# Performance work log

Hardware: AMD Instinct MI355X
Metric: run time of the kernel (lower is better)

Reference implementation:

```python
import jax, jax.numpy as jnp
import numpy as np
import math

JULIA_ITERS = 64
ESCAPE_RADIUS = 2.0


def _julia_escape_times(seq_len, c_real, c_imag):
    # Positions mapped to the real segment [-2, 2]; iterate z <- z^2 + c,
    # record (first iteration index where |z| > R) / ITERS, else 1.0.
    x = jnp.linspace(-2.0, 2.0, seq_len)
    zr0 = x
    zi0 = jnp.zeros_like(x)
    escaped0 = jnp.zeros(seq_len, dtype=bool)
    et0 = jnp.ones(seq_len, dtype=x.dtype)
    r2 = ESCAPE_RADIUS * ESCAPE_RADIUS

    def step(carry, it):
        zr, zi, escaped, et = carry
        nzr = zr * zr - zi * zi + c_real
        nzi = 2.0 * zr * zi + c_imag
        # torch breaks out of the loop once escaped -> freeze z afterwards
        zr = jnp.where(escaped, zr, nzr)
        zi = jnp.where(escaped, zi, nzi)
        mag2 = zr * zr + zi * zi
        newly = jnp.logical_and(~escaped, mag2 > r2)
        et = jnp.where(newly, it.astype(et.dtype) / JULIA_ITERS, et)
        escaped = jnp.logical_or(escaped, newly)
        return (zr, zi, escaped, et), None

    (_, _, _, et), _ = jax.lax.scan(step, (zr0, zi0, escaped0, et0), jnp.arange(JULIA_ITERS))
    return et


def setup_inputs() -> dict:
    key = jax.random.key(0)
    kq, kk, kv = jax.random.split(key, 3)
    B, S, D = 4, 8192, 64
    return {
        "query": jax.random.normal(kq, (B, S, D), dtype=jnp.float32),
        "key": jax.random.normal(kk, (B, S, D), dtype=jnp.float32),
        "value": jax.random.normal(kv, (B, S, D), dtype=jnp.float32),
        "julia_c_real": jnp.float32(-0.7),
        "julia_c_imag": jnp.float32(0.27),
        "escape_scale": jnp.float32(1.0),
    }


def reference(query, key, value, julia_c_real, julia_c_imag, escape_scale):
    B, S, D = key.shape
    et = _julia_escape_times(S, julia_c_real, julia_c_imag)            # [S]
    julia_weights = jnp.exp(et * escape_scale)                          # [S]
    bias = jnp.log(julia_weights + 1e-8)                                # [S]
    scores = jnp.einsum("bqd,bkd->bqk", query, key) / math.sqrt(D)     # [B,S,S]
    scores = scores + bias[None, None, :]
    attn = jax.nn.softmax(scores, axis=-1)
    out = jnp.einsum("bqk,bkd->bqd", attn, value)                       # [B,S,D]
    return out  # squeeze(1) is a no-op for S > 1
```

## Files before the change

### kernel.cpp

```cpp
#include <hip/hip_runtime.h>
#include <math.h>

#define S_LEN 8192
#define DHEAD 64
#define NBATCH 4
#define BK 32
#define KIT 64

typedef unsigned short u16;
typedef unsigned int u32;
typedef __attribute__((ext_vector_type(8))) _Float16 half8;
typedef __attribute__((ext_vector_type(2))) __fp16 fp16x2;
typedef __attribute__((ext_vector_type(4))) float f32x4;

union HU8 { int4 i4; half8 h8; u32 w[4]; };
union H2U { fp16x2 h2; u32 w; };
union HU  { _Float16 h; u16 u; };

#if __has_builtin(__builtin_amdgcn_exp2f)
#define EXP2(x) __builtin_amdgcn_exp2f(x)
#else
#define EXP2(x) exp2f(x)
#endif

__device__ __forceinline__ u16 f2h(float f) {
    HU x; x.h = (_Float16)f; return x.u;
}
__device__ __forceinline__ u32 packh2(float a, float b) {
    H2U x; x.h2 = __builtin_amdgcn_cvt_pkrtz(a, b); return x.w;
}

__global__ void prep_kernel(const float* __restrict__ K, const float* __restrict__ V,
                            const float* crp, const float* cip, const float* scp,
                            u16* __restrict__ blob, float* __restrict__ bias2) {
    int bid = blockIdx.x, tid = threadIdx.x;
    if (bid < 1024) {
        int b = bid >> 8, t = bid & 255;
        __shared__ float Kt[32 * 64];
        __shared__ float Vt[32 * 65];
        int row = tid >> 3, c8 = (tid & 7) * 8;
        const float* ks = K + ((size_t)(b * S_LEN + t * 32 + row)) * 64 + c8;
        const float* vs = V + ((size_t)(b * S_LEN + t * 32 + row)) * 64 + c8;
        float4 ka = *(const float4*)ks, kb4 = *(const float4*)(ks + 4);
        float4 va = *(const float4*)vs, vb4 = *(const float4*)(vs + 4);
        *(float4*)&Kt[row * 64 + c8] = ka;
        *(float4*)&Kt[row * 64 + c8 + 4] = kb4;
        float* vr = &Vt[row * 65 + c8];
        vr[0] = va.x; vr[1] = va.y; vr[2] = va.z; vr[3] = va.w;
        vr[4] = vb4.x; vr[5] = vb4.y; vr[6] = vb4.z; vr[7] = vb4.w;
        __syncthreads();

        int j = tid >> 6, lane = tid & 63, low = lane & 15, h = lane >> 4;
        u16* tb = blob + ((size_t)(b * 256 + t)) * 4096;
        {
            int kt = j >> 1, ds = j & 1;
            int krow = 8 * (low >> 2) + 4 * kt + (low & 3);
            const float* src = &Kt[krow * 64 + ds * 32 + h * 8];
            u32 wds[4];
#pragma unroll
            for (int i = 0; i < 4; ++i)
                wds[i] = (u32)f2h(src[2 * i]) | ((u32)f2h(src[2 * i + 1]) << 16);
            *(int4*)(tb + j * 512 + lane * 8) = make_int4(wds[0], wds[1], wds[2], wds[3]);
        }
        {
            int col = j * 16 + low;
            u32 wds[4];
#pragma unroll
            for (int i = 0; i < 4; ++i) {
                float a = Vt[(h * 8 + 2 * i) * 65 + col];
                float c = Vt[(h * 8 + 2 * i + 1) * 65 + col];
                wds[i] = (u32)f2h(a) | ((u32)f2h(c) << 16);
            }
            *(int4*)(tb + 2048 + j * 512 + lane * 8) = make_int4(wds[0], wds[1], wds[2], wds[3]);
        }
    } else {
#pragma clang fp contract(off)
        int i = (bid - 1024) * 256 + tid;
        double cr = (double)crp[0], ci = (double)cip[0], sc = (double)scp[0];
        double step = 4.0 / (double)(S_LEN - 1);
        double x = (i == S_LEN - 1) ? 2.0 : (-2.0 + step * (double)i);
        double zr = x, zi = 0.0, et = 1.0;
        bool esc = false;
        for (int it = 0; it < 64; ++it) {
            double nzr = zr * zr - zi * zi + cr;
            double nzi = 2.0 * zr * zi + ci;
            if (!esc) { zr = nzr; zi = nzi; }
            double m2 = zr * zr + zi * zi;
            if (!esc && m2 > 4.0) { et = (double)it / 64.0; esc = true; }
        }
        double bias = log(exp(et * sc) + 1e-8);
        bias2[i] = (float)(bias * 1.4426950408889634 - 20.0);
    }
}

__global__ __launch_bounds__(256, 2)
void flash_kernel(const float* __restrict__ Q, const u16* __restrict__ blob,
                  const float* __restrict__ bias2, float* __restrict__ Out) {
    __shared__ __align__(16) char smem[17664];

    const int tid = threadIdx.x;
    const int l = tid & 63, low = l & 15, h = l >> 4;
    const int kq = __builtin_amdgcn_readfirstlane(tid >> 6);

    const int bid = blockIdx.x;
    const int batch = bid & 3;
    const int qtile = bid >> 2;
    const int q0 = qtile * 64;

    const float qscale = 0.18033688011112042f;
    half8 qfrag[4][2];
#pragma unroll
    for (int qf = 0; qf < 4; ++qf) {
        const float* qrow = Q + ((size_t)(batch * S_LEN + q0 + qf * 16 + low)) * DHEAD + h * 8;
#pragma unroll
        for (int ds = 0; ds < 2; ++ds) {
            f32x4 a = *(const f32x4*)(qrow + ds * 32);
            f32x4 b = *(const f32x4*)(qrow + ds * 32 + 4);
            HU8 u;
            u.w[0] = packh2(a[0] * qscale, a[1] * qscale);
            u.w[1] = packh2(a[2] * qscale, a[3] * qscale);
            u.w[2] = packh2(b[0] * qscale, b[1] * qscale);
            u.w[3] = packh2(b[2] * qscale, b[3] * qscale);
            qfrag[qf][ds] = u.h8;
        }
    }

    const u16* kvb = blob + ((size_t)(batch * 256 + kq * 64)) * 4096;
    const int loff = l * 8;
    const float* bbase = bias2 + kq * 2048;

    f32x4 o[4][4];
#pragma unroll
    for (int qf = 0; qf < 4; ++qf)
#pragma unroll
        for (int dt = 0; dt < 4; ++dt) o[qf][dt] = (f32x4){0, 0, 0, 0};
    float lsum[4] = {0.f, 0.f, 0.f, 0.f};

    HU8 kf[2][4];
    f32x4 bvv[2][2];
#pragma unroll
    for (int j = 0; j < 4; ++j) kf[0][j].i4 = *(const int4*)(kvb + j * 512 + loff);
    bvv[0][0] = *(const f32x4*)(bbase + h * 8);
    bvv[0][1] = *(const f32x4*)(bbase + h * 8 + 4);

#pragma unroll 2
    for (int ki = 0; ki < KIT; ++ki) {
        const int c = ki & 1;
        const u16* tb = kvb + ki * 4096;

        HU8 vf[4];
#pragma unroll
        for (int j = 0; j < 4; ++j) vf[j].i4 = *(const int4*)(tb + 2048 + j * 512 + loff);

        const u16* tn = tb + 4096;
#pragma unroll
        for (int j = 0; j < 4; ++j) kf[c ^ 1][j].i4 = *(const int4*)(tn + j * 512 + loff);
        const float* bpn = bbase + (ki + 1) * 32 + h * 8;
        bvv[c ^ 1][0] = *(const f32x4*)bpn;
        bvv[c ^ 1][1] = *(const f32x4*)(bpn + 4);

        HU8 pf[4];
#pragma unroll
        for (int kt = 0; kt < 2; ++kt) {
            const f32x4 binit = kt ? bvv[c][1] : bvv[c][0];
            f32x4 st[4];
#pragma unroll
            for (int qf = 0; qf < 4; ++qf) {
                f32x4 a = __builtin_amdgcn_mfma_f32_16x16x32_f16(kf[c][kt * 2].h8, qfrag[qf][0], binit, 0, 0, 0);
                a = __builtin_amdgcn_mfma_f32_16x16x32_f16(kf[c][kt * 2 + 1].h8, qfrag[qf][1], a, 0, 0, 0);
                st[qf] = a;
            }
#pragma unroll
            for (int qf = 0; qf < 4; ++qf) {
                float p0 = EXP2(st[qf][0]), p1 = EXP2(st[qf][1]);
                float p2 = EXP2(st[qf][2]), p3 = EXP2(st[qf][3]);
                lsum[qf] += (p0 + p1) + (p2 + p3);
                pf[qf].w[kt * 2]     = packh2(p0, p1);
                pf[qf].w[kt * 2 + 1] = packh2(p2, p3);
            }
        }

#pragma unroll
        for (int dt = 0; dt < 4; ++dt)
#pragma unroll
            for (int qf = 0; qf < 4; ++qf)
                o[qf][dt] = __builtin_amdgcn_mfma_f32_16x16x32_f16(vf[dt].h8, pf[qf].h8, o[qf][dt], 0, 0, 0);
    }

#pragma unroll
    for (int qf = 0; qf < 4; ++qf) {
        lsum[qf] += __shfl_xor(lsum[qf], 16, 64);
        lsum[qf] += __shfl_xor(lsum[qf], 32, 64);
    }

    float* MO = (float*)smem;
    float* ML = (float*)(smem + 17408);
#pragma unroll 1
    for (int src = 1; src < 4; ++src) {
        __syncthreads();
        if (kq == src) {
#pragma unroll
            for (int qf = 0; qf < 4; ++qf) {
                const int row = qf * 16 + low;
#pragma unroll
                for (int dt = 0; dt < 4; ++dt)
                    *(f32x4*)&MO[row * 68 + dt * 16 + h * 4] = o[qf][dt];
                if (h == 0) ML[row] = lsum[qf];
            }
        }
        __syncthreads();
        if (kq == 0) {
#pragma unroll
            for (int qf = 0; qf < 4; ++qf) {
                const int row = qf * 16 + low;
#pragma unroll
                for (int dt = 0; dt < 4; ++dt) {
                    f32x4 a = *(const f32x4*)&MO[row * 68 + dt * 16 + h * 4];
#pragma unroll
                    for (int jj = 0; jj < 4; ++jj) o[qf][dt][jj] += a[jj];
                }
                lsum[qf] += ML[row];
            }
        }
    }

    if (kq == 0) {
#pragma unroll
        for (int qf = 0; qf < 4; ++qf) {
            const float inv = 1.f / lsum[qf];
            float* orow = Out + ((size_t)(batch * S_LEN + q0 + qf * 16 + low)) * DHEAD;
#pragma unroll
            for (int dt = 0; dt < 4; ++dt) {
                f32x4 r;
#pragma unroll
                for (int jj = 0; jj < 4; ++jj) r[jj] = o[qf][dt][jj] * inv;
                *(f32x4*)(orow + dt * 16 + h * 4) = r;
            }
        }
    }
}

extern "C" void kernel_launch(void* const* d_in, const int* in_sizes, int n_in,
                              void* d_out, int out_size, void* d_ws, size_t ws_size,
                              hipStream_t stream) {
    const float* Q  = (const float*)d_in[0];
    const float* K  = (const float*)d_in[1];
    const float* V  = (const float*)d_in[2];
    const float* cr = (const float*)d_in[3];
    const float* ci = (const float*)d_in[4];
    const float* sc = (const float*)d_in[5];
    float* out = (float*)d_out;

    char* ws = (char*)d_ws;
    float* bias2 = (float*)ws;
    u16*   blob  = (u16*)(ws + 32768);

    prep_kernel<<<dim3(1056), dim3(256), 0, stream>>>(K, V, cr, ci, sc, blob, bias2);
    flash_kernel<<<dim3(512), dim3(256), 0, stream>>>(Q, blob, bias2, out);
}
```

Measured before the change: 149.7 us.

## Split key range across eight waves per block with tree reduction

Doubles the block to 512 threads so eight waves each process half as many key tiles, raising in-block parallelism for the same 512-block grid. The serial three-step merge of partial outputs through shared memory is replaced by a log-depth tree reduction using a larger shared buffer. The larger shared footprint and register pressure under the new launch bounds may limit how many blocks fit per CU and could cause spills.

```diff
diff --git a/kernel.cpp b/kernel.cpp
--- a/kernel.cpp
+++ b/kernel.cpp
@@ -5,7 +5,7 @@
 #define DHEAD 64
 #define NBATCH 4
 #define BK 32
-#define KIT 64
+#define KIT 32
 
 typedef unsigned short u16;
 typedef unsigned int u32;
@@ -93,10 +93,10 @@
     }
 }
 
-__global__ __launch_bounds__(256, 2)
+__global__ __launch_bounds__(512, 4)
 void flash_kernel(const float* __restrict__ Q, const u16* __restrict__ blob,
                   const float* __restrict__ bias2, float* __restrict__ Out) {
-    __shared__ __align__(16) char smem[17664];
+    __shared__ __align__(16) char smem[70656];
 
     const int tid = threadIdx.x;
     const int l = tid & 63, low = l & 15, h = l >> 4;
@@ -125,9 +125,9 @@
         }
     }
 
-    const u16* kvb = blob + ((size_t)(batch * 256 + kq * 64)) * 4096;
+    const u16* kvb = blob + ((size_t)(batch * 256 + kq * 32)) * 4096;
     const int loff = l * 8;
-    const float* bbase = bias2 + kq * 2048;
+    const float* bbase = bias2 + kq * 1024;
 
     f32x4 o[4][4];
 #pragma unroll
@@ -194,37 +194,48 @@
     }
 
     float* MO = (float*)smem;
-    float* ML = (float*)(smem + 17408);
-#pragma unroll 1
-    for (int src = 1; src < 4; ++src) {
-        __syncthreads();
-        if (kq == src) {
-#pragma unroll
-            for (int qf = 0; qf < 4; ++qf) {
-                const int row = qf * 16 + low;
-#pragma unroll
-                for (int dt = 0; dt < 4; ++dt)
-                    *(f32x4*)&MO[row * 68 + dt * 16 + h * 4] = o[qf][dt];
-                if (h == 0) ML[row] = lsum[qf];
-            }
-        }
-        __syncthreads();
-        if (kq == 0) {
-#pragma unroll
-            for (int qf = 0; qf < 4; ++qf) {
-                const int row = qf * 16 + low;
-#pragma unroll
-                for (int dt = 0; dt < 4; ++dt) {
-                    f32x4 a = *(const f32x4*)&MO[row * 68 + dt * 16 + h * 4];
-#pragma unroll
-                    for (int jj = 0; jj < 4; ++jj) o[qf][dt][jj] += a[jj];
-                }
-                lsum[qf] += ML[row];
-            }
-        }
-    }
+    float* ML = (float*)(smem + 69632);
+#define WRITE_REGION(reg)                                                     \
+    do {                                                                      \
+        const int _r = (reg);                                                 \
+        _Pragma("unroll")                                                     \
+        for (int qf = 0; qf < 4; ++qf) {                                      \
+            const int row = qf * 16 + low;                                    \
+            _Pragma("unroll")                                                 \
+            for (int dt = 0; dt < 4; ++dt)                                    \
+                *(f32x4*)&MO[_r * 4352 + row * 68 + dt * 16 + h * 4] = o[qf][dt]; \
+            if (h == 0) ML[_r * 64 + row] = lsum[qf];                         \
+        }                                                                     \
+    } while (0)
+#define ADD_REGION(reg)                                                       \
+    do {                                                                      \
+        const int _r = (reg);                                                 \
+        _Pragma("unroll")                                                     \
+        for (int qf = 0; qf < 4; ++qf) {                                      \
+            const int row = qf * 16 + low;                                    \
+            _Pragma("unroll")                                                 \
+            for (int dt = 0; dt < 4; ++dt) {                                  \
+                f32x4 a = *(const f32x4*)&MO[_r * 4352 + row * 68 + dt * 16 + h * 4]; \
+                _Pragma("unroll")                                             \
+                for (int jj = 0; jj < 4; ++jj) o[qf][dt][jj] += a[jj];        \
+            }                                                                 \
+            lsum[qf] += ML[_r * 64 + row];                                    \
+        }                                                                     \
+    } while (0)
+
+    if (kq >= 4) WRITE_REGION(kq - 4);
+    __syncthreads();
+    if (kq < 4) ADD_REGION(kq);
+    __syncthreads();
+    if (kq == 2 || kq == 3) WRITE_REGION(kq - 2);
+    __syncthreads();
+    if (kq < 2) ADD_REGION(kq);
+    __syncthreads();
+    if (kq == 1) WRITE_REGION(0);
+    __syncthreads();
 
     if (kq == 0) {
+        ADD_REGION(0);
 #pragma unroll
         for (int qf = 0; qf < 4; ++qf) {
             const float inv = 1.f / lsum[qf];
@@ -238,6 +249,8 @@
             }
         }
     }
+#undef WRITE_REGION
+#undef ADD_REGION
 }
 
 extern "C" void kernel_launch(void* const* d_in, const int* in_sizes, int n_in,
@@ -256,5 +269,5 @@
     u16*   blob  = (u16*)(ws + 32768);
 
     prep_kernel<<<dim3(1056), dim3(256), 0, stream>>>(K, V, cr, ci, sc, blob, bias2);
-    flash_kernel<<<dim3(512), dim3(256), 0, stream>>>(Q, blob, bias2, out);
-}
+    flash_kernel<<<dim3(512), dim3(512), 0, stream>>>(Q, blob, bias2, out);
+}
```

New measurement: 569.9 us. +280.7%, slower.

## Split key range across two blocks per query tile and merge partials

Applied to the files above, without the earlier changes.

Doubles the grid so each block handles half the keys for a 64-query tile. Unnormalized partial outputs and row sums go to workspace, and a new merge kernel adds them and normalizes. This targets under-occupancy: 512 blocks at 2 per CU on 256 CUs fills only one wave. In exchange it adds extra global traffic for the partials (about 16 MB written and read) and a third kernel launch. The merge relies on a shared fixed max offset (bias minus 20 in log2 space) so partials can be summed without rescaling.

```diff
diff --git a/kernel.cpp b/kernel.cpp
--- a/kernel.cpp
+++ b/kernel.cpp
@@ -5,7 +5,7 @@
 #define DHEAD 64
 #define NBATCH 4
 #define BK 32
-#define KIT 64
+#define KIT 32
 
 typedef unsigned short u16;
 typedef unsigned int u32;
@@ -95,7 +95,8 @@
 
 __global__ __launch_bounds__(256, 2)
 void flash_kernel(const float* __restrict__ Q, const u16* __restrict__ blob,
-                  const float* __restrict__ bias2, float* __restrict__ Out) {
+                  const float* __restrict__ bias2, float* __restrict__ Ppart,
+                  float* __restrict__ Lpart) {
     __shared__ __align__(16) char smem[17664];
 
     const int tid = threadIdx.x;
@@ -104,7 +105,8 @@
 
     const int bid = blockIdx.x;
     const int batch = bid & 3;
-    const int qtile = bid >> 2;
+    const int khalf = (bid >> 2) & 1;
+    const int qtile = bid >> 3;
     const int q0 = qtile * 64;
 
     const float qscale = 0.18033688011112042f;
@@ -125,9 +127,9 @@
         }
     }
 
-    const u16* kvb = blob + ((size_t)(batch * 256 + kq * 64)) * 4096;
+    const u16* kvb = blob + ((size_t)(batch * 256 + khalf * 128 + kq * 32)) * 4096;
     const int loff = l * 8;
-    const float* bbase = bias2 + kq * 2048;
+    const float* bbase = bias2 + khalf * 4096 + kq * 1024;
 
     f32x4 o[4][4];
 #pragma unroll
@@ -225,19 +227,34 @@
     }
 
     if (kq == 0) {
+        float* pbase = Ppart + (size_t)khalf * (NBATCH * S_LEN * DHEAD);
+        float* lbase = Lpart + (size_t)khalf * (NBATCH * S_LEN);
 #pragma unroll
         for (int qf = 0; qf < 4; ++qf) {
-            const float inv = 1.f / lsum[qf];
-            float* orow = Out + ((size_t)(batch * S_LEN + q0 + qf * 16 + low)) * DHEAD;
-#pragma unroll
-            for (int dt = 0; dt < 4; ++dt) {
-                f32x4 r;
-#pragma unroll
-                for (int jj = 0; jj < 4; ++jj) r[jj] = o[qf][dt][jj] * inv;
-                *(f32x4*)(orow + dt * 16 + h * 4) = r;
-            }
-        }
-    }
+            const int row = q0 + qf * 16 + low;
+            float* prow = pbase + ((size_t)(batch * S_LEN + row)) * DHEAD;
+#pragma unroll
+            for (int dt = 0; dt < 4; ++dt)
+                *(f32x4*)(prow + dt * 16 + h * 4) = o[qf][dt];
+            if (h == 0) lbase[batch * S_LEN + row] = lsum[qf];
+        }
+    }
+}
+
+__global__ __launch_bounds__(256)
+void merge_kernel(const float* __restrict__ Ppart, const float* __restrict__ Lpart,
+                  float* __restrict__ Out) {
+    const size_t HALFP = (size_t)NBATCH * S_LEN * DHEAD;
+    size_t i = ((size_t)blockIdx.x * 256 + threadIdx.x) * 4;
+    int row = (int)(i >> 6);
+    f32x4 a = *(const f32x4*)(Ppart + i);
+    f32x4 b = *(const f32x4*)(Ppart + HALFP + i);
+    float lt = Lpart[row] + Lpart[NBATCH * S_LEN + row];
+    float inv = 1.0f / lt;
+    f32x4 r;
+#pragma unroll
+    for (int j = 0; j < 4; ++j) r[j] = (a[j] + b[j]) * inv;
+    *(f32x4*)(Out + i) = r;
 }
 
 extern "C" void kernel_launch(void* const* d_in, const int* in_sizes, int n_in,
@@ -254,7 +271,11 @@
     char* ws = (char*)d_ws;
     float* bias2 = (float*)ws;
     u16*   blob  = (u16*)(ws + 32768);
+    char*  after = ws + 32768 + 8388608 + 8192;
+    float* Ppart = (float*)after;
+    float* Lpart = (float*)(after + 2 * 8388608);
 
     prep_kernel<<<dim3(1056), dim3(256), 0, stream>>>(K, V, cr, ci, sc, blob, bias2);
-    flash_kernel<<<dim3(512), dim3(256), 0, stream>>>(Q, blob, bias2, out);
-}
+    flash_kernel<<<dim3(1024), dim3(256), 0, stream>>>(Q, blob, bias2, Ppart, Lpart);
+    merge_kernel<<<dim3((NBATCH * S_LEN * DHEAD) / 1024), dim3(256), 0, stream>>>(Ppart, Lpart, out);
+}
```

New measurement: 159.4 us. 1.07x slower.
